# Kernel optimization log

Measured on AMD Instinct MI355X. Metric: run time of the kernel, lower is better.

The kernel has to match this reference:

```python
import jax, jax.numpy as jnp
import numpy as np

X_DIM, Y_DIM, SEQ_LEN, BATCH = 50, 6, 230, 16384

def _dw_conv1d(x, w, b):
    # x: [B, C, L], w: [C, k], b: [C]; depthwise (groups=C) valid conv
    out = jax.lax.conv_general_dilated(
        x, w[:, None, :],  # rhs [C_out=C, C_in/groups=1, k]
        window_strides=(1,), padding='VALID',
        feature_group_count=x.shape[1],
        dimension_numbers=('NCW', 'OIW', 'NCW'))
    return out + b[None, :, None]

def setup_inputs() -> dict:
    key = jax.random.key(0)
    ks = jax.random.split(key, 9)
    f = lambda k, s, scale: (jax.random.normal(k, s, dtype=jnp.float32) * scale)
    return {
        'sequence': f(ks[0], (BATCH, SEQ_LEN, X_DIM), 1.0),
        'w1': f(ks[1], (X_DIM, 3), 1.0 / np.sqrt(3)),
        'b1': f(ks[2], (X_DIM,), 0.1),
        'w2': f(ks[3], (X_DIM, 6), 1.0 / np.sqrt(6)),
        'b2': f(ks[4], (X_DIM,), 0.1),
        'w3': f(ks[5], (X_DIM, 12), 1.0 / np.sqrt(12)),
        'b3': f(ks[6], (X_DIM,), 0.1),
        'w_out': f(ks[7], (Y_DIM * SEQ_LEN, 3 * X_DIM), 1.0 / np.sqrt(3 * X_DIM)),
        'b_out': f(ks[8], (Y_DIM * SEQ_LEN,), 0.1),
    }

def reference(sequence, w1, b1, w2, b2, w3, b3, w_out, b_out):
    # sequence: [B, 230, x_dim] -> [B, x_dim, 230]
    seq = jnp.transpose(sequence, (0, 2, 1))
    # Each conv+maxpool pair reduces to max over the full conv output length.
    m1 = jnp.max(_dw_conv1d(seq, w1, b1), axis=-1)  # [B, x_dim]
    m2 = jnp.max(_dw_conv1d(seq, w2, b2), axis=-1)
    m3 = jnp.max(_dw_conv1d(seq, w3, b3), axis=-1)
    # torch cat order is per-feature interleaved: (c1_f, c2_f, c3_f) for each f
    flat = jnp.stack([m1, m2, m3], axis=-1).reshape(seq.shape[0], 3 * X_DIM)
    out = flat @ w_out.T + b_out  # [B, y_dim*230]
    return out.reshape(-1, SEQ_LEN, Y_DIM)
```

## Files before the change

### kernel.cpp

```cpp
#include <hip/hip_runtime.h>
#include <math.h>

#define X_DIM   50
#define SEQ_LEN 230
#define BATCH   16384
#define KTRUE   150
#define KPAD    160
#define NOUT    1380
#define NPAD    1408

typedef float v2f __attribute__((ext_vector_type(2)));

__device__ __forceinline__ v2f vmax2(v2f a, v2f b) {
    v2f r; r.x = fmaxf(a.x, b.x); r.y = fmaxf(a.y, b.y); return r;
}

__global__ __launch_bounds__(256) void prep_w(const float* __restrict__ w,
                                              float* __restrict__ wp) {
    int i = blockIdx.x * 256 + threadIdx.x;
    int n = i / KPAD;
    int k = i - n * KPAD;
    float v = 0.f;
    if (n < NOUT && k < KTRUE) v = w[n * KTRUE + k];
    wp[i] = v;
}

__global__ __launch_bounds__(256) void conv_max(
    const float* __restrict__ x,
    const float* __restrict__ w1, const float* __restrict__ b1,
    const float* __restrict__ w2, const float* __restrict__ b2,
    const float* __restrict__ w3, const float* __restrict__ b3,
    float* __restrict__ flat) {
    int g = blockIdx.x * 256 + threadIdx.x;
    int b = g / 25;
    int cp = g - b * 25;
    int c0 = 2 * cp;
    int c1 = c0 + 1;

    const v2f* p = reinterpret_cast<const v2f*>(x + (size_t)b * (SEQ_LEN * X_DIM)) + cp;

    v2f W1c[3], W2c[6], W3c[12];
#pragma unroll
    for (int i = 0; i < 3; ++i)  { W1c[i].x = w1[c0 * 3 + i];  W1c[i].y = w1[c1 * 3 + i]; }
#pragma unroll
    for (int i = 0; i < 6; ++i)  { W2c[i].x = w2[c0 * 6 + i];  W2c[i].y = w2[c1 * 6 + i]; }
#pragma unroll
    for (int i = 0; i < 12; ++i) { W3c[i].x = w3[c0 * 12 + i]; W3c[i].y = w3[c1 * 12 + i]; }

    v2f m1 = {-1e30f, -1e30f}, m2 = m1, m3 = m1;
    v2f buf[12];

#pragma unroll
    for (int t = 0; t < 12; ++t) {
        v2f v = p[t * 25];
        buf[t] = v;
        if (t >= 2) {
            v2f s = buf[t - 2] * W1c[0] + buf[t - 1] * W1c[1] + v * W1c[2];
            m1 = vmax2(m1, s);
        }
        if (t >= 5) {
            v2f s = buf[t - 5] * W2c[0];
#pragma unroll
            for (int i = 1; i < 6; ++i) s += buf[t - 5 + i] * W2c[i];
            m2 = vmax2(m2, s);
        }
        if (t == 11) {
            v2f s = buf[0] * W3c[0];
#pragma unroll
            for (int i = 1; i < 12; ++i) s += buf[i] * W3c[i];
            m3 = vmax2(m3, s);
        }
    }

    const v2f* q = p + 12 * 25;
#pragma unroll 2
    for (int it = 0; it < 18; ++it) {
#pragma unroll
        for (int j = 0; j < 12; ++j) {
            v2f v = q[j * 25];
            buf[j] = v;
            v2f s1 = buf[(j + 10) % 12] * W1c[0] + buf[(j + 11) % 12] * W1c[1] + v * W1c[2];
            m1 = vmax2(m1, s1);
            v2f s2 = buf[(j + 7) % 12] * W2c[0];
#pragma unroll
            for (int i = 1; i < 6; ++i) s2 += buf[(j + 7 + i) % 12] * W2c[i];
            m2 = vmax2(m2, s2);
            v2f s3 = buf[(j + 1) % 12] * W3c[0];
#pragma unroll
            for (int i = 1; i < 12; ++i) s3 += buf[(j + 1 + i) % 12] * W3c[i];
            m3 = vmax2(m3, s3);
        }
        q += 12 * 25;
    }

#pragma unroll
    for (int j = 0; j < 2; ++j) {
        v2f v = q[j * 25];
        buf[j] = v;
        v2f s1 = buf[(j + 10) % 12] * W1c[0] + buf[(j + 11) % 12] * W1c[1] + v * W1c[2];
        m1 = vmax2(m1, s1);
        v2f s2 = buf[(j + 7) % 12] * W2c[0];
#pragma unroll
        for (int i = 1; i < 6; ++i) s2 += buf[(j + 7 + i) % 12] * W2c[i];
        m2 = vmax2(m2, s2);
        v2f s3 = buf[(j + 1) % 12] * W3c[0];
#pragma unroll
        for (int i = 1; i < 12; ++i) s3 += buf[(j + 1 + i) % 12] * W3c[i];
        m3 = vmax2(m3, s3);
    }

    size_t base = (size_t)b * KPAD + 6 * cp;
    flat[base + 0] = m1.x + b1[c0];
    flat[base + 1] = m2.x + b2[c0];
    flat[base + 2] = m3.x + b3[c0];
    flat[base + 3] = m1.y + b1[c1];
    flat[base + 4] = m2.y + b2[c1];
    flat[base + 5] = m3.y + b3[c1];
    if (cp < KPAD - KTRUE) flat[(size_t)b * KPAD + KTRUE + cp] = 0.f;
}

#define BM 128
#define BN 128
#define BK 16
#define NCHUNK (KPAD / BK)

__global__ __launch_bounds__(256) void gemm_k(
    const float* __restrict__ A,
    const float* __restrict__ Wp,
    const float* __restrict__ bias,
    float* __restrict__ out) {
    __shared__ float As[2][BK][BM];
    __shared__ float Bs[2][BK][BN];

    int tid = threadIdx.x;
    int bn = blockIdx.x * BN;
    int bm = blockIdx.y * BM;
    int tm = tid >> 4;
    int tn = tid & 15;

    int lrow = tid >> 2;
    int lk4  = (tid & 3) * 4;

    const float* Ap = A  + (size_t)(bm + lrow) * KPAD + lk4;
    const float* Bp = Wp + (size_t)(bn + lrow) * KPAD + lk4;

    float acc[8][8] = {};

    {
        float4 a0  = *(const float4*)(Ap);
        float4 a1  = *(const float4*)(Ap + (size_t)64 * KPAD);
        float4 c0  = *(const float4*)(Bp);
        float4 c1  = *(const float4*)(Bp + (size_t)64 * KPAD);
        As[0][lk4 + 0][lrow] = a0.x;  As[0][lk4 + 1][lrow] = a0.y;
        As[0][lk4 + 2][lrow] = a0.z;  As[0][lk4 + 3][lrow] = a0.w;
        As[0][lk4 + 0][lrow + 64] = a1.x;  As[0][lk4 + 1][lrow + 64] = a1.y;
        As[0][lk4 + 2][lrow + 64] = a1.z;  As[0][lk4 + 3][lrow + 64] = a1.w;
        Bs[0][lk4 + 0][lrow] = c0.x;  Bs[0][lk4 + 1][lrow] = c0.y;
        Bs[0][lk4 + 2][lrow] = c0.z;  Bs[0][lk4 + 3][lrow] = c0.w;
        Bs[0][lk4 + 0][lrow + 64] = c1.x;  Bs[0][lk4 + 1][lrow + 64] = c1.y;
        Bs[0][lk4 + 2][lrow + 64] = c1.z;  Bs[0][lk4 + 3][lrow + 64] = c1.w;
        __syncthreads();
    }

    for (int k0 = 0; k0 < NCHUNK; ++k0) {
        int cur = k0 & 1;

        float4 a0, a1, c0, c1;
        if (k0 < NCHUNK - 1) {
            int off = (k0 + 1) * BK;
            a0 = *(const float4*)(Ap + off);
            a1 = *(const float4*)(Ap + (size_t)64 * KPAD + off);
            c0 = *(const float4*)(Bp + off);
            c1 = *(const float4*)(Bp + (size_t)64 * KPAD + off);
        }

#pragma unroll
        for (int k = 0; k < BK; ++k) {
            float4 av0 = *(const float4*)&As[cur][k][tm * 8];
            float4 av1 = *(const float4*)&As[cur][k][tm * 8 + 4];
            float4 bv0 = *(const float4*)&Bs[cur][k][tn * 4];
            float4 bv1 = *(const float4*)&Bs[cur][k][tn * 4 + 64];
            float a[8]  = {av0.x, av0.y, av0.z, av0.w, av1.x, av1.y, av1.z, av1.w};
            float bf[8] = {bv0.x, bv0.y, bv0.z, bv0.w, bv1.x, bv1.y, bv1.z, bv1.w};
#pragma unroll
            for (int i = 0; i < 8; ++i)
#pragma unroll
                for (int jj = 0; jj < 8; ++jj)
                    acc[i][jj] = fmaf(a[i], bf[jj], acc[i][jj]);
        }

        if (k0 < NCHUNK - 1) {
            int nxt = cur ^ 1;
            As[nxt][lk4 + 0][lrow] = a0.x;  As[nxt][lk4 + 1][lrow] = a0.y;
            As[nxt][lk4 + 2][lrow] = a0.z;  As[nxt][lk4 + 3][lrow] = a0.w;
            As[nxt][lk4 + 0][lrow + 64] = a1.x;  As[nxt][lk4 + 1][lrow + 64] = a1.y;
            As[nxt][lk4 + 2][lrow + 64] = a1.z;  As[nxt][lk4 + 3][lrow + 64] = a1.w;
            Bs[nxt][lk4 + 0][lrow] = c0.x;  Bs[nxt][lk4 + 1][lrow] = c0.y;
            Bs[nxt][lk4 + 2][lrow] = c0.z;  Bs[nxt][lk4 + 3][lrow] = c0.w;
            Bs[nxt][lk4 + 0][lrow + 64] = c1.x;  Bs[nxt][lk4 + 1][lrow + 64] = c1.y;
            Bs[nxt][lk4 + 2][lrow + 64] = c1.z;  Bs[nxt][lk4 + 3][lrow + 64] = c1.w;
            __syncthreads();
        }
    }

#pragma unroll
    for (int i = 0; i < 8; ++i) {
        size_t m = (size_t)(bm + tm * 8 + i);
        int n0 = bn + tn * 4;
        float4 r0;
        r0.x = acc[i][0] + bias[n0 + 0];
        r0.y = acc[i][1] + bias[n0 + 1];
        r0.z = acc[i][2] + bias[n0 + 2];
        r0.w = acc[i][3] + bias[n0 + 3];
        *(float4*)(out + m * NOUT + n0) = r0;
        int n1 = bn + 64 + tn * 4;
        if (n1 < NOUT) {
            float4 r1;
            r1.x = acc[i][4] + bias[n1 + 0];
            r1.y = acc[i][5] + bias[n1 + 1];
            r1.z = acc[i][6] + bias[n1 + 2];
            r1.w = acc[i][7] + bias[n1 + 3];
            *(float4*)(out + m * NOUT + n1) = r1;
        }
    }
}

extern "C" void kernel_launch(void* const* d_in, const int* in_sizes, int n_in,
                              void* d_out, int out_size, void* d_ws, size_t ws_size,
                              hipStream_t stream) {
    const float* seq   = (const float*)d_in[0];
    const float* w1    = (const float*)d_in[1];
    const float* b1    = (const float*)d_in[2];
    const float* w2    = (const float*)d_in[3];
    const float* b2    = (const float*)d_in[4];
    const float* w3    = (const float*)d_in[5];
    const float* b3    = (const float*)d_in[6];
    const float* w_out = (const float*)d_in[7];
    const float* b_out = (const float*)d_in[8];
    float* out = (float*)d_out;

    float* flat = (float*)d_ws;
    float* wp   = flat + (size_t)BATCH * KPAD;

    prep_w<<<(NPAD * KPAD) / 256, 256, 0, stream>>>(w_out, wp);
    conv_max<<<(BATCH * 25) / 256, 256, 0, stream>>>(
        seq, w1, b1, w2, b2, w3, b3, flat);
    gemm_k<<<dim3(NPAD / BN, BATCH / BM), 256, 0, stream>>>(flat, wp, b_out, out);
}
```

Before: 1.129 ms.

## Fuse depthwise conv-max and output GEMM into one per-batch-tile kernel

Replaces the three kernels (weight padding, conv+max to a global flat buffer, tiled GEMM) with one kernel. Each block handles 8 batch rows: 200 threads compute the conv maxima into shared memory, then all 256 threads each produce up to 6 output columns for those 8 rows, streaming w_out directly from global memory. This removes the flat buffer round trip and the extra launches. In exchange the GEMM loses tiled reuse of w_out: every block re-reads the whole weight matrix from cache, the K loop reads uncoalesced rows, and 56 threads sit idle during the conv phase.

```diff
diff --git a/kernel.cpp b/kernel.cpp
--- a/kernel.cpp
+++ b/kernel.cpp
@@ -5,9 +5,10 @@
 #define SEQ_LEN 230
 #define BATCH   16384
 #define KTRUE   150
-#define KPAD    160
 #define NOUT    1380
-#define NPAD    1408
+#define BM      8
+#define FSTR    156
+#define NCOLS   6
 
 typedef float v2f __attribute__((ext_vector_type(2)));
 
@@ -15,212 +16,181 @@
     v2f r; r.x = fmaxf(a.x, b.x); r.y = fmaxf(a.y, b.y); return r;
 }
 
-__global__ __launch_bounds__(256) void prep_w(const float* __restrict__ w,
-                                              float* __restrict__ wp) {
-    int i = blockIdx.x * 256 + threadIdx.x;
-    int n = i / KPAD;
-    int k = i - n * KPAD;
-    float v = 0.f;
-    if (n < NOUT && k < KTRUE) v = w[n * KTRUE + k];
-    wp[i] = v;
-}
-
-__global__ __launch_bounds__(256) void conv_max(
+__global__ __launch_bounds__(256) void fused_cnn(
     const float* __restrict__ x,
     const float* __restrict__ w1, const float* __restrict__ b1,
     const float* __restrict__ w2, const float* __restrict__ b2,
     const float* __restrict__ w3, const float* __restrict__ b3,
-    float* __restrict__ flat) {
-    int g = blockIdx.x * 256 + threadIdx.x;
-    int b = g / 25;
-    int cp = g - b * 25;
-    int c0 = 2 * cp;
-    int c1 = c0 + 1;
-
-    const v2f* p = reinterpret_cast<const v2f*>(x + (size_t)b * (SEQ_LEN * X_DIM)) + cp;
-
-    v2f W1c[3], W2c[6], W3c[12];
-#pragma unroll
-    for (int i = 0; i < 3; ++i)  { W1c[i].x = w1[c0 * 3 + i];  W1c[i].y = w1[c1 * 3 + i]; }
-#pragma unroll
-    for (int i = 0; i < 6; ++i)  { W2c[i].x = w2[c0 * 6 + i];  W2c[i].y = w2[c1 * 6 + i]; }
-#pragma unroll
-    for (int i = 0; i < 12; ++i) { W3c[i].x = w3[c0 * 12 + i]; W3c[i].y = w3[c1 * 12 + i]; }
-
-    v2f m1 = {-1e30f, -1e30f}, m2 = m1, m3 = m1;
-    v2f buf[12];
-
-#pragma unroll
-    for (int t = 0; t < 12; ++t) {
-        v2f v = p[t * 25];
-        buf[t] = v;
-        if (t >= 2) {
-            v2f s = buf[t - 2] * W1c[0] + buf[t - 1] * W1c[1] + v * W1c[2];
-            m1 = vmax2(m1, s);
-        }
-        if (t >= 5) {
-            v2f s = buf[t - 5] * W2c[0];
-#pragma unroll
-            for (int i = 1; i < 6; ++i) s += buf[t - 5 + i] * W2c[i];
-            m2 = vmax2(m2, s);
-        }
-        if (t == 11) {
-            v2f s = buf[0] * W3c[0];
-#pragma unroll
-            for (int i = 1; i < 12; ++i) s += buf[i] * W3c[i];
-            m3 = vmax2(m3, s);
-        }
-    }
-
-    const v2f* q = p + 12 * 25;
+    const float* __restrict__ wo,
+    const float* __restrict__ bo,
+    float* __restrict__ out)
+{
+    __shared__ float flatS[BM * FSTR];
+
+    const int tid = threadIdx.x;
+    const int b0  = blockIdx.x * BM;
+
+    if (tid < BM * 25) {
+        const int lb = tid / 25;
+        const int cp = tid - lb * 25;
+        const int c0 = 2 * cp, c1 = c0 + 1;
+
+        const v2f* p = reinterpret_cast<const v2f*>(
+            x + (size_t)(b0 + lb) * (SEQ_LEN * X_DIM)) + cp;
+
+        v2f W1c[3], W2c[6], W3c[12];
+#pragma unroll
+        for (int i = 0; i < 3; ++i)  { W1c[i].x = w1[c0*3+i];  W1c[i].y = w1[c1*3+i]; }
+#pragma unroll
+        for (int i = 0; i < 6; ++i)  { W2c[i].x = w2[c0*6+i];  W2c[i].y = w2[c1*6+i]; }
+#pragma unroll
+        for (int i = 0; i < 12; ++i) { W3c[i].x = w3[c0*12+i]; W3c[i].y = w3[c1*12+i]; }
+
+        v2f m1 = {-1e30f, -1e30f}, m2 = m1, m3 = m1;
+        v2f buf[12];
+
+#pragma unroll
+        for (int t = 0; t < 12; ++t) {
+            v2f v = p[t * 25];
+            buf[t] = v;
+            if (t >= 2) {
+                v2f s = buf[t-2] * W1c[0] + buf[t-1] * W1c[1] + v * W1c[2];
+                m1 = vmax2(m1, s);
+            }
+            if (t >= 5) {
+                v2f s = buf[t-5] * W2c[0];
+#pragma unroll
+                for (int i = 1; i < 6; ++i) s += buf[t-5+i] * W2c[i];
+                m2 = vmax2(m2, s);
+            }
+            if (t == 11) {
+                v2f s = buf[0] * W3c[0];
+#pragma unroll
+                for (int i = 1; i < 12; ++i) s += buf[i] * W3c[i];
+                m3 = vmax2(m3, s);
+            }
+        }
+
+        const v2f* q = p + 12 * 25;
 #pragma unroll 2
-    for (int it = 0; it < 18; ++it) {
-#pragma unroll
-        for (int j = 0; j < 12; ++j) {
+        for (int it = 0; it < 18; ++it) {
+#pragma unroll
+            for (int j = 0; j < 12; ++j) {
+                v2f v = q[j * 25];
+                buf[j] = v;
+                v2f s1 = buf[(j+10)%12] * W1c[0] + buf[(j+11)%12] * W1c[1] + v * W1c[2];
+                m1 = vmax2(m1, s1);
+                v2f s2 = buf[(j+7)%12] * W2c[0];
+#pragma unroll
+                for (int i = 1; i < 6; ++i) s2 += buf[(j+7+i)%12] * W2c[i];
+                m2 = vmax2(m2, s2);
+                v2f s3 = buf[(j+1)%12] * W3c[0];
+#pragma unroll
+                for (int i = 1; i < 12; ++i) s3 += buf[(j+1+i)%12] * W3c[i];
+                m3 = vmax2(m3, s3);
+            }
+            q += 12 * 25;
+        }
+
+#pragma unroll
+        for (int j = 0; j < 2; ++j) {
             v2f v = q[j * 25];
             buf[j] = v;
-            v2f s1 = buf[(j + 10) % 12] * W1c[0] + buf[(j + 11) % 12] * W1c[1] + v * W1c[2];
+            v2f s1 = buf[(j+10)%12] * W1c[0] + buf[(j+11)%12] * W1c[1] + v * W1c[2];
             m1 = vmax2(m1, s1);
-            v2f s2 = buf[(j + 7) % 12] * W2c[0];
-#pragma unroll
-            for (int i = 1; i < 6; ++i) s2 += buf[(j + 7 + i) % 12] * W2c[i];
+            v2f s2 = buf[(j+7)%12] * W2c[0];
+#pragma unroll
+            for (int i = 1; i < 6; ++i) s2 += buf[(j+7+i)%12] * W2c[i];
             m2 = vmax2(m2, s2);
-            v2f s3 = buf[(j + 1) % 12] * W3c[0];
-#pragma unroll
-            for (int i = 1; i < 12; ++i) s3 += buf[(j + 1 + i) % 12] * W3c[i];
+            v2f s3 = buf[(j+1)%12] * W3c[0];
+#pragma unroll
+            for (int i = 1; i < 12; ++i) s3 += buf[(j+1+i)%12] * W3c[i];
             m3 = vmax2(m3, s3);
         }
-        q += 12 * 25;
-    }
-
-#pragma unroll
-    for (int j = 0; j < 2; ++j) {
-        v2f v = q[j * 25];
-        buf[j] = v;
-        v2f s1 = buf[(j + 10) % 12] * W1c[0] + buf[(j + 11) % 12] * W1c[1] + v * W1c[2];
-        m1 = vmax2(m1, s1);
-        v2f s2 = buf[(j + 7) % 12] * W2c[0];
-#pragma unroll
-        for (int i = 1; i < 6; ++i) s2 += buf[(j + 7 + i) % 12] * W2c[i];
-        m2 = vmax2(m2, s2);
-        v2f s3 = buf[(j + 1) % 12] * W3c[0];
-#pragma unroll
-        for (int i = 1; i < 12; ++i) s3 += buf[(j + 1 + i) % 12] * W3c[i];
-        m3 = vmax2(m3, s3);
-    }
-
-    size_t base = (size_t)b * KPAD + 6 * cp;
-    flat[base + 0] = m1.x + b1[c0];
-    flat[base + 1] = m2.x + b2[c0];
-    flat[base + 2] = m3.x + b3[c0];
-    flat[base + 3] = m1.y + b1[c1];
-    flat[base + 4] = m2.y + b2[c1];
-    flat[base + 5] = m3.y + b3[c1];
-    if (cp < KPAD - KTRUE) flat[(size_t)b * KPAD + KTRUE + cp] = 0.f;
-}
-
-#define BM 128
-#define BN 128
-#define BK 16
-#define NCHUNK (KPAD / BK)
-
-__global__ __launch_bounds__(256) void gemm_k(
-    const float* __restrict__ A,
-    const float* __restrict__ Wp,
-    const float* __restrict__ bias,
-    float* __restrict__ out) {
-    __shared__ float As[2][BK][BM];
-    __shared__ float Bs[2][BK][BN];
-
-    int tid = threadIdx.x;
-    int bn = blockIdx.x * BN;
-    int bm = blockIdx.y * BM;
-    int tm = tid >> 4;
-    int tn = tid & 15;
-
-    int lrow = tid >> 2;
-    int lk4  = (tid & 3) * 4;
-
-    const float* Ap = A  + (size_t)(bm + lrow) * KPAD + lk4;
-    const float* Bp = Wp + (size_t)(bn + lrow) * KPAD + lk4;
-
-    float acc[8][8] = {};
+
+        float* f = flatS + lb * FSTR + 6 * cp;
+        f[0] = m1.x + b1[c0];
+        f[1] = m2.x + b2[c0];
+        f[2] = m3.x + b3[c0];
+        f[3] = m1.y + b1[c1];
+        f[4] = m2.y + b2[c1];
+        f[5] = m3.y + b3[c1];
+    }
+    __syncthreads();
+
+    const float* wp_[NCOLS];
+#pragma unroll
+    for (int j = 0; j < NCOLS; ++j) {
+        int n = tid + 256 * j;
+        if (n > NOUT - 1) n = NOUT - 1;
+        wp_[j] = wo + (size_t)n * KTRUE;
+    }
+
+    float acc[NCOLS][BM];
+#pragma unroll
+    for (int j = 0; j < NCOLS; ++j)
+#pragma unroll
+        for (int r = 0; r < BM; ++r) acc[j][r] = 0.f;
+
+#pragma unroll 1
+    for (int kb = 0; kb < 18; ++kb) {
+        const int k0 = kb * 8;
+        v2f wreg[NCOLS][4];
+#pragma unroll
+        for (int j = 0; j < NCOLS; ++j)
+#pragma unroll
+            for (int qq = 0; qq < 4; ++qq)
+                wreg[j][qq] = *reinterpret_cast<const v2f*>(wp_[j] + k0 + 2*qq);
+
+#pragma unroll
+        for (int r = 0; r < BM; ++r) {
+            float4 aa = *reinterpret_cast<const float4*>(&flatS[r*FSTR + k0]);
+            float4 ab = *reinterpret_cast<const float4*>(&flatS[r*FSTR + k0 + 4]);
+            float av[8] = {aa.x, aa.y, aa.z, aa.w, ab.x, ab.y, ab.z, ab.w};
+#pragma unroll
+            for (int j = 0; j < NCOLS; ++j) {
+#pragma unroll
+                for (int qq = 0; qq < 4; ++qq) {
+                    acc[j][r] = fmaf(av[2*qq+0], wreg[j][qq].x, acc[j][r]);
+                    acc[j][r] = fmaf(av[2*qq+1], wreg[j][qq].y, acc[j][r]);
+                }
+            }
+        }
+    }
 
     {
-        float4 a0  = *(const float4*)(Ap);
-        float4 a1  = *(const float4*)(Ap + (size_t)64 * KPAD);
-        float4 c0  = *(const float4*)(Bp);
-        float4 c1  = *(const float4*)(Bp + (size_t)64 * KPAD);
-        As[0][lk4 + 0][lrow] = a0.x;  As[0][lk4 + 1][lrow] = a0.y;
-        As[0][lk4 + 2][lrow] = a0.z;  As[0][lk4 + 3][lrow] = a0.w;
-        As[0][lk4 + 0][lrow + 64] = a1.x;  As[0][lk4 + 1][lrow + 64] = a1.y;
-        As[0][lk4 + 2][lrow + 64] = a1.z;  As[0][lk4 + 3][lrow + 64] = a1.w;
-        Bs[0][lk4 + 0][lrow] = c0.x;  Bs[0][lk4 + 1][lrow] = c0.y;
-        Bs[0][lk4 + 2][lrow] = c0.z;  Bs[0][lk4 + 3][lrow] = c0.w;
-        Bs[0][lk4 + 0][lrow + 64] = c1.x;  Bs[0][lk4 + 1][lrow + 64] = c1.y;
-        Bs[0][lk4 + 2][lrow + 64] = c1.z;  Bs[0][lk4 + 3][lrow + 64] = c1.w;
-        __syncthreads();
-    }
-
-    for (int k0 = 0; k0 < NCHUNK; ++k0) {
-        int cur = k0 & 1;
-
-        float4 a0, a1, c0, c1;
-        if (k0 < NCHUNK - 1) {
-            int off = (k0 + 1) * BK;
-            a0 = *(const float4*)(Ap + off);
-            a1 = *(const float4*)(Ap + (size_t)64 * KPAD + off);
-            c0 = *(const float4*)(Bp + off);
-            c1 = *(const float4*)(Bp + (size_t)64 * KPAD + off);
-        }
-
-#pragma unroll
-        for (int k = 0; k < BK; ++k) {
-            float4 av0 = *(const float4*)&As[cur][k][tm * 8];
-            float4 av1 = *(const float4*)&As[cur][k][tm * 8 + 4];
-            float4 bv0 = *(const float4*)&Bs[cur][k][tn * 4];
-            float4 bv1 = *(const float4*)&Bs[cur][k][tn * 4 + 64];
-            float a[8]  = {av0.x, av0.y, av0.z, av0.w, av1.x, av1.y, av1.z, av1.w};
-            float bf[8] = {bv0.x, bv0.y, bv0.z, bv0.w, bv1.x, bv1.y, bv1.z, bv1.w};
-#pragma unroll
-            for (int i = 0; i < 8; ++i)
-#pragma unroll
-                for (int jj = 0; jj < 8; ++jj)
-                    acc[i][jj] = fmaf(a[i], bf[jj], acc[i][jj]);
-        }
-
-        if (k0 < NCHUNK - 1) {
-            int nxt = cur ^ 1;
-            As[nxt][lk4 + 0][lrow] = a0.x;  As[nxt][lk4 + 1][lrow] = a0.y;
-            As[nxt][lk4 + 2][lrow] = a0.z;  As[nxt][lk4 + 3][lrow] = a0.w;
-            As[nxt][lk4 + 0][lrow + 64] = a1.x;  As[nxt][lk4 + 1][lrow + 64] = a1.y;
-            As[nxt][lk4 + 2][lrow + 64] = a1.z;  As[nxt][lk4 + 3][lrow + 64] = a1.w;
-            Bs[nxt][lk4 + 0][lrow] = c0.x;  Bs[nxt][lk4 + 1][lrow] = c0.y;
-            Bs[nxt][lk4 + 2][lrow] = c0.z;  Bs[nxt][lk4 + 3][lrow] = c0.w;
-            Bs[nxt][lk4 + 0][lrow + 64] = c1.x;  Bs[nxt][lk4 + 1][lrow + 64] = c1.y;
-            Bs[nxt][lk4 + 2][lrow + 64] = c1.z;  Bs[nxt][lk4 + 3][lrow + 64] = c1.w;
-            __syncthreads();
-        }
-    }
-
-#pragma unroll
-    for (int i = 0; i < 8; ++i) {
-        size_t m = (size_t)(bm + tm * 8 + i);
-        int n0 = bn + tn * 4;
-        float4 r0;
-        r0.x = acc[i][0] + bias[n0 + 0];
-        r0.y = acc[i][1] + bias[n0 + 1];
-        r0.z = acc[i][2] + bias[n0 + 2];
-        r0.w = acc[i][3] + bias[n0 + 3];
-        *(float4*)(out + m * NOUT + n0) = r0;
-        int n1 = bn + 64 + tn * 4;
-        if (n1 < NOUT) {
-            float4 r1;
-            r1.x = acc[i][4] + bias[n1 + 0];
-            r1.y = acc[i][5] + bias[n1 + 1];
-            r1.z = acc[i][6] + bias[n1 + 2];
-            r1.w = acc[i][7] + bias[n1 + 3];
-            *(float4*)(out + m * NOUT + n1) = r1;
+        const int k0 = 144;
+        v2f wreg[NCOLS][3];
+#pragma unroll
+        for (int j = 0; j < NCOLS; ++j)
+#pragma unroll
+            for (int qq = 0; qq < 3; ++qq)
+                wreg[j][qq] = *reinterpret_cast<const v2f*>(wp_[j] + k0 + 2*qq);
+
+#pragma unroll
+        for (int r = 0; r < BM; ++r) {
+            float4 aa = *reinterpret_cast<const float4*>(&flatS[r*FSTR + k0]);
+            v2f    ab = *reinterpret_cast<const v2f*>(&flatS[r*FSTR + k0 + 4]);
+            float av[6] = {aa.x, aa.y, aa.z, aa.w, ab.x, ab.y};
+#pragma unroll
+            for (int j = 0; j < NCOLS; ++j) {
+#pragma unroll
+                for (int qq = 0; qq < 3; ++qq) {
+                    acc[j][r] = fmaf(av[2*qq+0], wreg[j][qq].x, acc[j][r]);
+                    acc[j][r] = fmaf(av[2*qq+1], wreg[j][qq].y, acc[j][r]);
+                }
+            }
+        }
+    }
+
+#pragma unroll
+    for (int j = 0; j < NCOLS; ++j) {
+        int n = tid + 256 * j;
+        if (n < NOUT) {
+            float bb = bo[n];
+#pragma unroll
+            for (int r = 0; r < BM; ++r)
+                out[(size_t)(b0 + r) * NOUT + n] = acc[j][r] + bb;
         }
     }
 }
@@ -239,11 +209,8 @@
     const float* b_out = (const float*)d_in[8];
     float* out = (float*)d_out;
 
-    float* flat = (float*)d_ws;
-    float* wp   = flat + (size_t)BATCH * KPAD;
-
-    prep_w<<<(NPAD * KPAD) / 256, 256, 0, stream>>>(w_out, wp);
-    conv_max<<<(BATCH * 25) / 256, 256, 0, stream>>>(
-        seq, w1, b1, w2, b2, w3, b3, flat);
-    gemm_k<<<dim3(NPAD / BN, BATCH / BM), 256, 0, stream>>>(flat, wp, b_out, out);
+    (void)d_ws; (void)ws_size;
+
+    fused_cnn<<<BATCH / BM, 256, 0, stream>>>(
+        seq, w1, b1, w2, b2, w3, b3, w_out, b_out, out);
 }
```

Measured after the change: 1.260 ms. 11.6% more time.
